# Performance work log

Hardware: AMD Instinct MI355X
Metric: run time of the kernel (lower is better)

The kernel has to match this reference:

```python
import jax, jax.numpy as jnp
import numpy as np


def _count_components(img, cls):
    """Count 4-connected components of pixels equal to `cls` in a 2D int map.

    Equivalent to the numba DFS flood fill: each component is counted once.
    Implemented as min-label propagation: seed every in-class pixel with its
    linear index, iterate min over 4-neighbors (same-class only, since
    out-of-class pixels hold the sentinel BIG) until convergence; a component
    root is a pixel whose final label equals its own index.
    """
    H, W = img.shape
    BIG = H * W  # sentinel larger than any pixel index
    mask = img == cls
    idx = jnp.arange(BIG, dtype=jnp.int32).reshape(H, W)
    lab0 = jnp.where(mask, idx, BIG).astype(jnp.int32)

    def cond(state):
        return state[1]

    def body(state):
        lab, _ = state
        p = jnp.pad(lab, 1, constant_values=BIG)
        nmin = jnp.minimum(jnp.minimum(p[:-2, 1:-1], p[2:, 1:-1]),
                           jnp.minimum(p[1:-1, :-2], p[1:-1, 2:]))
        new = jnp.where(mask, jnp.minimum(lab, nmin), BIG)
        return new, jnp.any(new != lab)

    lab, _ = jax.lax.while_loop(cond, body, (lab0, jnp.array(True)))
    # roots: in-class pixels whose propagated label is their own index
    return jnp.sum(mask & (lab == idx)).astype(jnp.float32)


def _counts23(img):
    # component counts for labels 2 and 3 (the only ones the loss uses)
    return _count_components(img, 2), _count_components(img, 3)


def setup_inputs() -> dict:
    key = jax.random.key(0)
    k1, k2 = jax.random.split(key)
    pred = jax.random.normal(k1, (8, 4, 1, 768, 768), dtype=jnp.float32)
    anno = jax.random.randint(k2, (8, 1, 768, 768), 0, 4, dtype=jnp.int32)
    return {"pred": pred, "anno": anno}


def reference(pred, anno):
    # pred: [B, C, 1, H, W], anno: [B, 1, H, W]
    pred_argmax = jnp.argmax(pred, axis=1)[:, 0]  # [B, H, W] (detached semantics)
    anno_map = anno[:, 0]                          # [B, H, W]
    a2, a3 = jax.vmap(_counts23)(anno_map)
    p2, p3 = jax.vmap(_counts23)(pred_argmax)
    term2 = 1.0 - 2.0 * jnp.minimum(p2, a2) / (a2 + p2)
    term3 = 1.0 - 2.0 * jnp.minimum(p3, a3) / (a3 + p3)
    # original sums per-batch terms into connEF, then loss = connEF / 2
    return jnp.sum(term2 + term3) / 2.0
```

## Files before the change

kernel.cpp:

```cpp
#include <hip/hip_runtime.h>

#define W     768
#define PIX   (768*768)
#define NMAPS 16
#define TROWS 6
#define TPX   (TROWS*W)
#define NT    (768/TROWS)
#define NB    (NT-1)
#define NSEG  (TPX/64)
#define NIT   (NSEG/4)
#define CSLOT 16


__device__ __forceinline__ int find_root_p(volatile int* L, int x) {
    int y = L[x] >> 2;
    while (y != x) { x = y; y = L[x] >> 2; }
    return x;
}

__device__ __forceinline__ bool unite_p(int* L, int a, int b, int c) {
    volatile int* Lv = L;
    while (true) {
        a = find_root_p(Lv, a);
        b = find_root_p(Lv, b);
        if (a == b) return false;
        if (a > b) { int t = a; a = b; b = t; }
        int old = atomicMin(&L[b], (a << 2) | c);
        if ((old >> 2) == b) return true;
        b = old >> 2;
    }
}


__global__ __launch_bounds__(256) void fused_k(const float* __restrict__ pred,
                                               const int*   __restrict__ anno,
                                               int* __restrict__ labels,
                                               int* __restrict__ counts, int m0) {
    __shared__ int lab[TPX];
    __shared__ int s2[4], s3[4];

    int mc   = blockIdx.x / NT;
    int t    = blockIdx.x - mc * NT;
    int m    = m0 + mc;
    int tid  = threadIdx.x;
    int wid  = tid >> 6;
    int lane = tid & 63;

    unsigned long long lem = (lane == 63) ? ~0ULL : ((2ULL << lane) - 1);

    int pc[3] = {0, 0, 0};
    int pm[3] = {0, 0, 0};
    int c2 = 0, c3 = 0;

    const int*   asrc = anno + (size_t)m * PIX + (size_t)t * TPX;
    const float* psrc = pred + (size_t)(m < 8 ? 0 : (m - 8)) * 4 * PIX + (size_t)t * TPX;
    bool is_anno = (m < 8);

    int   na = 0;
    float nv0 = 0.f, nv1 = 0.f, nv2 = 0.f, nv3 = 0.f;
    {
        int px = wid * 64 + lane;
        if (is_anno) {
            na = asrc[px];
        } else {
            nv0 = psrc[px];
            nv1 = psrc[(size_t)PIX + px];
            nv2 = psrc[(size_t)2 * PIX + px];
            nv3 = psrc[(size_t)3 * PIX + px];
        }
    }

    #pragma unroll
    for (int it = 0; it < NIT; ++it) {
        int seg = wid + 4 * it;
        int px  = seg * 64 + lane;
        int   ca = na;
        float v0 = nv0, v1 = nv1, v2 = nv2, v3 = nv3;
        if (it + 1 < NIT) {
            int pxn = px + 256;
            if (is_anno) {
                na = asrc[pxn];
            } else {
                nv0 = psrc[pxn];
                nv1 = psrc[(size_t)PIX + pxn];
                nv2 = psrc[(size_t)2 * PIX + pxn];
                nv3 = psrc[(size_t)3 * PIX + pxn];
            }
        }
        int c;
        if (is_anno) {
            c = ca & 3;
        } else {
            c = 0; float bv = v0;
            if (v1 > bv) { bv = v1; c = 1; }
            if (v2 > bv) { bv = v2; c = 2; }
            if (v3 > bv) { bv = v3; c = 3; }
        }
        unsigned long long blo = __ballot(c & 1);
        unsigned long long bhi = __ballot(c & 2);
        unsigned long long dif = ((blo ^ (blo << 1)) | (bhi ^ (bhi << 1))) | 1ULL;
        if (lane == 0) {
            c2 += (int)__popcll(dif & bhi & ~blo);
            c3 += (int)__popcll(dif & bhi &  blo);
        }
        int ms = 63 - __clzll(dif & lem);
        lab[px] = ((seg * 64 + ms) << 2) | c;
        const int sl = it % 3;
        if (it >= 3) {
            if ((c & 2) && c == pc[sl]) {
                int mx = ms > pm[sl] ? ms : pm[sl];
                if (lane == mx && unite_p(lab, px - W, px, c)) {
                    if (c == 2) c2--; else c3--;
                }
            }
        }
        pc[sl] = c; pm[sl] = ms;
    }
    __syncthreads();

    if (tid < TROWS * 11) {
        int row = tid / 11, j = tid % 11;
        int px  = row * W + (j + 1) * 64;
        int v = lab[px], c = v & 3;
        if (c & 2) {
            int vl = lab[px - 1];
            if ((vl & 3) == c && unite_p(lab, px - 1, px, c)) {
                if (c == 2) c2--; else c3--;
            }
        }
    }
    __syncthreads();

    int lbase = t * TPX;
    int* gl = labels + (size_t)mc * PIX + lbase;
    #pragma unroll
    for (int q = 0; q < 6; ++q) {
        int it  = (q < 3) ? q : (NIT - 6 + q);
        int seg = wid + 4 * it;
        int px  = seg * 64 + lane;
        int v   = lab[px];
        int c   = v & 3;
        int r   = px;
        if (c & 2) r = find_root_p(lab, px);
        int rl = __shfl_up(r, 1);
        gl[px] = ((lbase + r) << 2) | c;
        if ((c & 2) && (lane == 0 || rl != r))
            gl[r] = ((lbase + r) << 2) | c;
    }
    for (int off = 32; off; off >>= 1) {
        c2 += __shfl_down(c2, off, 64);
        c3 += __shfl_down(c3, off, 64);
    }
    if (lane == 0) { s2[wid] = c2; s3[wid] = c3; }
    __syncthreads();
    if (tid == 0) {
        int t2 = s2[0] + s2[1] + s2[2] + s2[3];
        int t3 = s3[0] + s3[1] + s3[2] + s3[3];
        if (t2) atomicAdd(&counts[(m * 2 + 0) * CSLOT], t2);
        if (t3) atomicAdd(&counts[(m * 2 + 1) * CSLOT], t3);
    }
}

__global__ __launch_bounds__(256) void boundary_k(int* __restrict__ labels,
                                                  int* __restrict__ counts, int m0) {
    __shared__ int s2[4], s3[4];
    const int HM = NB * (W / 2);
    int i    = blockIdx.x * 256 + threadIdx.x;
    int mc   = blockIdx.y;
    int m    = m0 + mc;
    int lane = threadIdx.x & 63;

    int m2 = 0, m3 = 0;
    if (i < HM) {
        int b   = i / (W / 2);
        int col = (i - b * (W / 2)) * 2;
        int* L  = labels + (size_t)mc * PIX;
        int p1  = b * TPX + (TROWS - 1) * W + col;
        int p2  = p1 + W;
        int2 va = *(const int2*)&L[p1];
        int2 vb = *(const int2*)&L[p2];
        int pay = __shfl_up(va.y, 1), pby = __shfl_up(vb.y, 1);
        int c0 = va.x & 3;
        if (c0 == (vb.x & 3) && (c0 & 2)) {
            bool red = (lane > 0) && (pay == va.x) && (pby == vb.x);
            if (!red && unite_p(L, p1, p2, c0)) { if (c0 == 2) m2++; else m3++; }
        }
        int c1 = va.y & 3;
        if (c1 == (vb.y & 3) && (c1 & 2)) {
            bool red = (va.x == va.y) && (vb.x == vb.y);
            if (!red && unite_p(L, p1 + 1, p2 + 1, c1)) { if (c1 == 2) m2++; else m3++; }
        }
    }
    for (int off = 32; off; off >>= 1) {
        m2 += __shfl_down(m2, off, 64);
        m3 += __shfl_down(m3, off, 64);
    }
    int wid = threadIdx.x >> 6;
    if (lane == 0) { s2[wid] = m2; s3[wid] = m3; }
    __syncthreads();
    if (threadIdx.x == 0) {
        int t2 = s2[0] + s2[1] + s2[2] + s2[3];
        int t3 = s3[0] + s3[1] + s3[2] + s3[3];
        if (t2) atomicSub(&counts[(m * 2 + 0) * CSLOT], t2);
        if (t3) atomicSub(&counts[(m * 2 + 1) * CSLOT], t3);
    }
}

__global__ void final_k(const int* __restrict__ counts, float* __restrict__ out) {
    float s = 0.0f;
    for (int b = 0; b < 8; ++b) {
        float a2 = (float)counts[(b * 2 + 0) * CSLOT];
        float a3 = (float)counts[(b * 2 + 1) * CSLOT];
        float p2 = (float)counts[((8 + b) * 2 + 0) * CSLOT];
        float p3 = (float)counts[((8 + b) * 2 + 1) * CSLOT];
        float t2 = 1.0f - 2.0f * fminf(p2, a2) / (a2 + p2);
        float t3 = 1.0f - 2.0f * fminf(p3, a3) / (a3 + p3);
        s += t2 + t3;
    }
    out[0] = 0.5f * s;
}


extern "C" void kernel_launch(void* const* d_in, const int* in_sizes, int n_in,
                              void* d_out, int out_size, void* d_ws, size_t ws_size,
                              hipStream_t stream) {
    const float* pred = (const float*)d_in[0];
    const int*   anno = (const int*)d_in[1];
    float* out = (float*)d_out;

    int* counts = (int*)d_ws;
    char* base  = (char*)d_ws + 4096;

    const size_t per_map = (size_t)PIX * 4;
    size_t avail = (ws_size > 4096) ? ws_size - 4096 : 0;
    int K = (int)(avail / per_map);
    if (K > NMAPS) K = NMAPS;
    if (K < 1)     K = 1;

    hipMemsetAsync(counts, 0, 32 * CSLOT * sizeof(int), stream);

    const int HM = NB * (W / 2);
    for (int m0 = 0; m0 < NMAPS; m0 += K) {
        int nm = NMAPS - m0; if (nm > K) nm = K;
        int* labels = (int*)base;
        fused_k   <<<dim3(nm * NT), 256, 0, stream>>>(pred, anno, labels, counts, m0);
        boundary_k<<<dim3((HM + 255) / 256, nm), 256, 0, stream>>>(labels, counts, m0);
    }
    final_k<<<1, 1, 0, stream>>>(counts, out);
}
```

Before: 59.51 us.

## Remap fused CCL tile so each lane handles two pixels in 128-wide row strips

The fused labeling kernel now runs 384 threads, one wave per 128-pixel column strip. Each lane loads two adjacent pixels per row with int2/float2 vector loads and iterates down the 6 rows. Run-start detection combines two ballots per pair, and vertical unions now link consecutive rows within the same wave, with no 3-slot history. The change aims to widen memory accesses, halve the number of ballot iterations and reduce seam unions (5 per row instead of 11). It adds more complex run-boundary logic, and the two-pixels-per-lane indexing is a possible source of correctness bugs.

```diff
diff --git a/kernel.cpp b/kernel.cpp
--- a/kernel.cpp
+++ b/kernel.cpp
@@ -7,8 +7,7 @@
 #define TPX   (TROWS*W)
 #define NT    (768/TROWS)
 #define NB    (NT-1)
-#define NSEG  (TPX/64)
-#define NIT   (NSEG/4)
+#define SW    128
 #define CSLOT 16
 
 
@@ -32,12 +31,12 @@
 }
 
 
-__global__ __launch_bounds__(256) void fused_k(const float* __restrict__ pred,
+__global__ __launch_bounds__(384) void fused_k(const float* __restrict__ pred,
                                                const int*   __restrict__ anno,
                                                int* __restrict__ labels,
                                                int* __restrict__ counts, int m0) {
     __shared__ int lab[TPX];
-    __shared__ int s2[4], s3[4];
+    __shared__ int s2[6], s3[6];
 
     int mc   = blockIdx.x / NT;
     int t    = blockIdx.x - mc * NT;
@@ -47,80 +46,100 @@
     int lane = tid & 63;
 
     unsigned long long lem = (lane == 63) ? ~0ULL : ((2ULL << lane) - 1);
-
-    int pc[3] = {0, 0, 0};
-    int pm[3] = {0, 0, 0};
+    unsigned long long ltm = lem ^ (1ULL << lane);
+
+    int pc0 = 0, pc1 = 0;
+    int pr0 = 0, pr1 = 0;
     int c2 = 0, c3 = 0;
 
     const int*   asrc = anno + (size_t)m * PIX + (size_t)t * TPX;
     const float* psrc = pred + (size_t)(m < 8 ? 0 : (m - 8)) * 4 * PIX + (size_t)t * TPX;
     bool is_anno = (m < 8);
 
-    int   na = 0;
-    float nv0 = 0.f, nv1 = 0.f, nv2 = 0.f, nv3 = 0.f;
-    {
-        int px = wid * 64 + lane;
+    int sp = wid * SW + 2 * lane;
+
+    int2   na = make_int2(0, 0);
+    float2 nv0 = {0,0}, nv1 = {0,0}, nv2 = {0,0}, nv3 = {0,0};
+    if (is_anno) {
+        na = *(const int2*)&asrc[sp];
+    } else {
+        const float2* f = (const float2*)psrc;
+        int i2 = sp >> 1;
+        nv0 = f[i2];
+        nv1 = f[(PIX >> 1) + i2];
+        nv2 = f[2 * (PIX >> 1) + i2];
+        nv3 = f[3 * (PIX >> 1) + i2];
+    }
+
+    #pragma unroll
+    for (int r = 0; r < TROWS; ++r) {
+        int tb  = r * W + wid * SW;
+        int px0 = tb + 2 * lane;
+        int2   ca = na;
+        float2 v0 = nv0, v1 = nv1, v2 = nv2, v3 = nv3;
+        if (r + 1 < TROWS) {
+            int spn = px0 + W;
+            if (is_anno) {
+                na = *(const int2*)&asrc[spn];
+            } else {
+                const float2* f = (const float2*)psrc;
+                int i2 = spn >> 1;
+                nv0 = f[i2];
+                nv1 = f[(PIX >> 1) + i2];
+                nv2 = f[2 * (PIX >> 1) + i2];
+                nv3 = f[3 * (PIX >> 1) + i2];
+            }
+        }
+        int c0, c1;
         if (is_anno) {
-            na = asrc[px];
+            c0 = ca.x & 3; c1 = ca.y & 3;
         } else {
-            nv0 = psrc[px];
-            nv1 = psrc[(size_t)PIX + px];
-            nv2 = psrc[(size_t)2 * PIX + px];
-            nv3 = psrc[(size_t)3 * PIX + px];
-        }
-    }
-
-    #pragma unroll
-    for (int it = 0; it < NIT; ++it) {
-        int seg = wid + 4 * it;
-        int px  = seg * 64 + lane;
-        int   ca = na;
-        float v0 = nv0, v1 = nv1, v2 = nv2, v3 = nv3;
-        if (it + 1 < NIT) {
-            int pxn = px + 256;
-            if (is_anno) {
-                na = asrc[pxn];
-            } else {
-                nv0 = psrc[pxn];
-                nv1 = psrc[(size_t)PIX + pxn];
-                nv2 = psrc[(size_t)2 * PIX + pxn];
-                nv3 = psrc[(size_t)3 * PIX + pxn];
-            }
-        }
-        int c;
-        if (is_anno) {
-            c = ca & 3;
-        } else {
-            c = 0; float bv = v0;
-            if (v1 > bv) { bv = v1; c = 1; }
-            if (v2 > bv) { bv = v2; c = 2; }
-            if (v3 > bv) { bv = v3; c = 3; }
-        }
-        unsigned long long blo = __ballot(c & 1);
-        unsigned long long bhi = __ballot(c & 2);
-        unsigned long long dif = ((blo ^ (blo << 1)) | (bhi ^ (bhi << 1))) | 1ULL;
+            {   float bv = v0.x; c0 = 0;
+                if (v1.x > bv) { bv = v1.x; c0 = 1; }
+                if (v2.x > bv) { bv = v2.x; c0 = 2; }
+                if (v3.x > bv) { bv = v3.x; c0 = 3; } }
+            {   float bv = v0.y; c1 = 0;
+                if (v1.y > bv) { bv = v1.y; c1 = 1; }
+                if (v2.y > bv) { bv = v2.y; c1 = 2; }
+                if (v3.y > bv) { bv = v3.y; c1 = 3; } }
+        }
+        unsigned long long blo0 = __ballot(c0 & 1);
+        unsigned long long bhi0 = __ballot(c0 & 2);
+        unsigned long long blo1 = __ballot(c1 & 1);
+        unsigned long long bhi1 = __ballot(c1 & 2);
+        unsigned long long d0 = ((blo0 ^ (blo1 << 1)) | (bhi0 ^ (bhi1 << 1))) | 1ULL;
+        unsigned long long d1 = (blo1 ^ blo0) | (bhi1 ^ bhi0);
         if (lane == 0) {
-            c2 += (int)__popcll(dif & bhi & ~blo);
-            c3 += (int)__popcll(dif & bhi &  blo);
-        }
-        int ms = 63 - __clzll(dif & lem);
-        lab[px] = ((seg * 64 + ms) << 2) | c;
-        const int sl = it % 3;
-        if (it >= 3) {
-            if ((c & 2) && c == pc[sl]) {
-                int mx = ms > pm[sl] ? ms : pm[sl];
-                if (lane == mx && unite_p(lab, px - W, px, c)) {
-                    if (c == 2) c2--; else c3--;
+            c2 += (int)__popcll(d0 & bhi0 & ~blo0) + (int)__popcll(d1 & bhi1 & ~blo1);
+            c3 += (int)__popcll(d0 & bhi0 &  blo0) + (int)__popcll(d1 & bhi1 &  blo1);
+        }
+        int rs0 = 2 * (63 - __clzll(d0 & lem));
+        unsigned long long mm = d1 & ltm;
+        if (mm) { int q = 2 * (63 - __clzll(mm)) + 1; if (q > rs0) rs0 = q; }
+        int rs1 = ((d1 >> lane) & 1) ? 2 * lane + 1 : rs0;
+        *(int2*)&lab[px0] = make_int2(((tb + rs0) << 2) | c0,
+                                      ((tb + rs1) << 2) | c1);
+        if (r > 0) {
+            if ((c0 & 2) && c0 == pc0) {
+                int mx = rs0 > pr0 ? rs0 : pr0;
+                if (mx == 2 * lane && unite_p(lab, px0 - W, px0, c0)) {
+                    if (c0 == 2) c2--; else c3--;
                 }
             }
-        }
-        pc[sl] = c; pm[sl] = ms;
-    }
-    __syncthreads();
-
-    if (tid < TROWS * 11) {
-        int row = tid / 11, j = tid % 11;
-        int px  = row * W + (j + 1) * 64;
+            if ((c1 & 2) && c1 == pc1) {
+                int mx = rs1 > pr1 ? rs1 : pr1;
+                if (mx == 2 * lane + 1 && unite_p(lab, px0 + 1 - W, px0 + 1, c1)) {
+                    if (c1 == 2) c2--; else c3--;
+                }
+            }
+        }
+        pc0 = c0; pc1 = c1; pr0 = rs0; pr1 = rs1;
+    }
+    __syncthreads();
+
+    if (tid < TROWS * 5) {
+        int row = tid / 5, s = tid % 5 + 1;
+        int px  = row * W + s * SW;
         int v = lab[px], c = v & 3;
         if (c & 2) {
             int vl = lab[px - 1];
@@ -134,18 +153,20 @@
     int lbase = t * TPX;
     int* gl = labels + (size_t)mc * PIX + lbase;
     #pragma unroll
-    for (int q = 0; q < 6; ++q) {
-        int it  = (q < 3) ? q : (NIT - 6 + q);
-        int seg = wid + 4 * it;
-        int px  = seg * 64 + lane;
-        int v   = lab[px];
-        int c   = v & 3;
-        int r   = px;
-        if (c & 2) r = find_root_p(lab, px);
-        int rl = __shfl_up(r, 1);
-        gl[px] = ((lbase + r) << 2) | c;
-        if ((c & 2) && (lane == 0 || rl != r))
-            gl[r] = ((lbase + r) << 2) | c;
+    for (int q = 0; q < 2; ++q) {
+        int r   = q ? (TROWS - 1) : 0;
+        int px0 = r * W + wid * SW + 2 * lane;
+        int v0 = lab[px0], v1 = lab[px0 + 1];
+        int c0 = v0 & 3, c1 = v1 & 3;
+        int r0 = (c0 & 2) ? find_root_p(lab, px0)     : px0;
+        int r1 = (c1 & 2) ? find_root_p(lab, px0 + 1) : px0 + 1;
+        *(int2*)&gl[px0] = make_int2(((lbase + r0) << 2) | c0,
+                                     ((lbase + r1) << 2) | c1);
+        int rl = __shfl_up(r1, 1);
+        if ((c0 & 2) && (lane == 0 || rl != r0))
+            gl[r0] = ((lbase + r0) << 2) | c0;
+        if ((c1 & 2) && r1 != r0)
+            gl[r1] = ((lbase + r1) << 2) | c1;
     }
     for (int off = 32; off; off >>= 1) {
         c2 += __shfl_down(c2, off, 64);
@@ -154,8 +175,8 @@
     if (lane == 0) { s2[wid] = c2; s3[wid] = c3; }
     __syncthreads();
     if (tid == 0) {
-        int t2 = s2[0] + s2[1] + s2[2] + s2[3];
-        int t3 = s3[0] + s3[1] + s3[2] + s3[3];
+        int t2 = s2[0] + s2[1] + s2[2] + s2[3] + s2[4] + s2[5];
+        int t3 = s3[0] + s3[1] + s3[2] + s3[3] + s3[4] + s3[5];
         if (t2) atomicAdd(&counts[(m * 2 + 0) * CSLOT], t2);
         if (t3) atomicAdd(&counts[(m * 2 + 1) * CSLOT], t3);
     }
@@ -243,7 +264,7 @@
     for (int m0 = 0; m0 < NMAPS; m0 += K) {
         int nm = NMAPS - m0; if (nm > K) nm = K;
         int* labels = (int*)base;
-        fused_k   <<<dim3(nm * NT), 256, 0, stream>>>(pred, anno, labels, counts, m0);
+        fused_k   <<<dim3(nm * NT), 384, 0, stream>>>(pred, anno, labels, counts, m0);
         boundary_k<<<dim3((HM + 255) / 256, nm), 256, 0, stream>>>(labels, counts, m0);
     }
     final_k<<<1, 1, 0, stream>>>(counts, out);
```

Result: slower. 62.90 us (+5.7%).

## Split fused kernel into specialized anno and pred kernels with different tile heights

Applied to the files above, without the earlier changes.

Replaces the single fused labeling kernel, which branched per map between the int annotation path and the 4-channel float argmax path, with two specialized kernels. The annotation kernel keeps 6-row tiles, while the prediction kernel uses 3-row tiles so more blocks share the heavier 4-channel loads. The boundary merge kernel is templated on tile height. Maps are now processed in two separate batches of at most 8, which doubles the launches when the workspace could hold all 16 maps, and 3-row pred tiles add more boundary rows to merge.

```diff
diff --git a/kernel.cpp b/kernel.cpp
--- a/kernel.cpp
+++ b/kernel.cpp
@@ -2,14 +2,16 @@
 
 #define W     768
 #define PIX   (768*768)
-#define NMAPS 16
-#define TROWS 6
-#define TPX   (TROWS*W)
-#define NT    (768/TROWS)
-#define NB    (NT-1)
-#define NSEG  (TPX/64)
-#define NIT   (NSEG/4)
 #define CSLOT 16
+
+#define TR_A  6
+#define TPX_A (TR_A*W)
+#define NT_A  (768/TR_A)
+#define NIT_A 18
+#define TR_P  3
+#define TPX_P (TR_P*W)
+#define NT_P  (768/TR_P)
+#define NIT_P 9
 
 
 __device__ __forceinline__ int find_root_p(volatile int* L, int x) {
@@ -32,92 +34,11 @@
 }
 
 
-__global__ __launch_bounds__(256) void fused_k(const float* __restrict__ pred,
-                                               const int*   __restrict__ anno,
-                                               int* __restrict__ labels,
-                                               int* __restrict__ counts, int m0) {
-    __shared__ int lab[TPX];
-    __shared__ int s2[4], s3[4];
-
-    int mc   = blockIdx.x / NT;
-    int t    = blockIdx.x - mc * NT;
-    int m    = m0 + mc;
-    int tid  = threadIdx.x;
-    int wid  = tid >> 6;
-    int lane = tid & 63;
-
-    unsigned long long lem = (lane == 63) ? ~0ULL : ((2ULL << lane) - 1);
-
-    int pc[3] = {0, 0, 0};
-    int pm[3] = {0, 0, 0};
-    int c2 = 0, c3 = 0;
-
-    const int*   asrc = anno + (size_t)m * PIX + (size_t)t * TPX;
-    const float* psrc = pred + (size_t)(m < 8 ? 0 : (m - 8)) * 4 * PIX + (size_t)t * TPX;
-    bool is_anno = (m < 8);
-
-    int   na = 0;
-    float nv0 = 0.f, nv1 = 0.f, nv2 = 0.f, nv3 = 0.f;
-    {
-        int px = wid * 64 + lane;
-        if (is_anno) {
-            na = asrc[px];
-        } else {
-            nv0 = psrc[px];
-            nv1 = psrc[(size_t)PIX + px];
-            nv2 = psrc[(size_t)2 * PIX + px];
-            nv3 = psrc[(size_t)3 * PIX + px];
-        }
-    }
-
-    #pragma unroll
-    for (int it = 0; it < NIT; ++it) {
-        int seg = wid + 4 * it;
-        int px  = seg * 64 + lane;
-        int   ca = na;
-        float v0 = nv0, v1 = nv1, v2 = nv2, v3 = nv3;
-        if (it + 1 < NIT) {
-            int pxn = px + 256;
-            if (is_anno) {
-                na = asrc[pxn];
-            } else {
-                nv0 = psrc[pxn];
-                nv1 = psrc[(size_t)PIX + pxn];
-                nv2 = psrc[(size_t)2 * PIX + pxn];
-                nv3 = psrc[(size_t)3 * PIX + pxn];
-            }
-        }
-        int c;
-        if (is_anno) {
-            c = ca & 3;
-        } else {
-            c = 0; float bv = v0;
-            if (v1 > bv) { bv = v1; c = 1; }
-            if (v2 > bv) { bv = v2; c = 2; }
-            if (v3 > bv) { bv = v3; c = 3; }
-        }
-        unsigned long long blo = __ballot(c & 1);
-        unsigned long long bhi = __ballot(c & 2);
-        unsigned long long dif = ((blo ^ (blo << 1)) | (bhi ^ (bhi << 1))) | 1ULL;
-        if (lane == 0) {
-            c2 += (int)__popcll(dif & bhi & ~blo);
-            c3 += (int)__popcll(dif & bhi &  blo);
-        }
-        int ms = 63 - __clzll(dif & lem);
-        lab[px] = ((seg * 64 + ms) << 2) | c;
-        const int sl = it % 3;
-        if (it >= 3) {
-            if ((c & 2) && c == pc[sl]) {
-                int mx = ms > pm[sl] ? ms : pm[sl];
-                if (lane == mx && unite_p(lab, px - W, px, c)) {
-                    if (c == 2) c2--; else c3--;
-                }
-            }
-        }
-        pc[sl] = c; pm[sl] = ms;
-    }
-    __syncthreads();
-
+template <int TROWS, int NIT>
+__device__ __forceinline__ void tile_tail(int* lab, int* labels, int* counts,
+                                          int mc, int t, int m,
+                                          int tid, int wid, int lane,
+                                          int c2, int c3, int* s2, int* s3) {
     if (tid < TROWS * 11) {
         int row = tid / 11, j = tid % 11;
         int px  = row * W + (j + 1) * 64;
@@ -131,7 +52,7 @@
     }
     __syncthreads();
 
-    int lbase = t * TPX;
+    int lbase = t * (TROWS * W);
     int* gl = labels + (size_t)mc * PIX + lbase;
     #pragma unroll
     for (int q = 0; q < 6; ++q) {
@@ -161,9 +82,125 @@
     }
 }
 
+__global__ __launch_bounds__(256) void anno_k(const int* __restrict__ anno,
+                                              int* __restrict__ labels,
+                                              int* __restrict__ counts, int m0) {
+    __shared__ int lab[TPX_A];
+    __shared__ int s2[4], s3[4];
+    int mc   = blockIdx.x / NT_A;
+    int t    = blockIdx.x - mc * NT_A;
+    int m    = m0 + mc;
+    int tid  = threadIdx.x;
+    int wid  = tid >> 6;
+    int lane = tid & 63;
+    unsigned long long lem = (lane == 63) ? ~0ULL : ((2ULL << lane) - 1);
+
+    int pc[3] = {0,0,0}, pm[3] = {0,0,0};
+    int c2 = 0, c3 = 0;
+    const int* asrc = anno + (size_t)m * PIX + (size_t)t * TPX_A;
+
+    int na = asrc[wid * 64 + lane];
+    #pragma unroll
+    for (int it = 0; it < NIT_A; ++it) {
+        int seg = wid + 4 * it;
+        int px  = seg * 64 + lane;
+        int ca  = na;
+        if (it + 1 < NIT_A) na = asrc[px + 256];
+        int c = ca & 3;
+        unsigned long long blo = __ballot(c & 1);
+        unsigned long long bhi = __ballot(c & 2);
+        unsigned long long dif = ((blo ^ (blo << 1)) | (bhi ^ (bhi << 1))) | 1ULL;
+        if (lane == 0) {
+            c2 += (int)__popcll(dif & bhi & ~blo);
+            c3 += (int)__popcll(dif & bhi &  blo);
+        }
+        int ms = 63 - __clzll(dif & lem);
+        lab[px] = ((seg * 64 + ms) << 2) | c;
+        const int sl = it % 3;
+        if (it >= 3) {
+            if ((c & 2) && c == pc[sl]) {
+                int mx = ms > pm[sl] ? ms : pm[sl];
+                if (lane == mx && unite_p(lab, px - W, px, c)) {
+                    if (c == 2) c2--; else c3--;
+                }
+            }
+        }
+        pc[sl] = c; pm[sl] = ms;
+    }
+    __syncthreads();
+    tile_tail<TR_A, NIT_A>(lab, labels, counts, mc, t, m, tid, wid, lane, c2, c3, s2, s3);
+}
+
+__global__ __launch_bounds__(256) void pred_k(const float* __restrict__ pred,
+                                              int* __restrict__ labels,
+                                              int* __restrict__ counts, int m0) {
+    __shared__ int lab[TPX_P];
+    __shared__ int s2[4], s3[4];
+    int mc   = blockIdx.x / NT_P;
+    int t    = blockIdx.x - mc * NT_P;
+    int m    = m0 + mc;
+    int tid  = threadIdx.x;
+    int wid  = tid >> 6;
+    int lane = tid & 63;
+    unsigned long long lem = (lane == 63) ? ~0ULL : ((2ULL << lane) - 1);
+
+    int pc[3] = {0,0,0}, pm[3] = {0,0,0};
+    int c2 = 0, c3 = 0;
+    const float* psrc = pred + (size_t)(m - 8) * 4 * PIX + (size_t)t * TPX_P;
+
+    float nv0, nv1, nv2, nv3;
+    {
+        int px = wid * 64 + lane;
+        nv0 = psrc[px];
+        nv1 = psrc[(size_t)PIX + px];
+        nv2 = psrc[(size_t)2 * PIX + px];
+        nv3 = psrc[(size_t)3 * PIX + px];
+    }
+    #pragma unroll
+    for (int it = 0; it < NIT_P; ++it) {
+        int seg = wid + 4 * it;
+        int px  = seg * 64 + lane;
+        float v0 = nv0, v1 = nv1, v2 = nv2, v3 = nv3;
+        if (it + 1 < NIT_P) {
+            int pxn = px + 256;
+            nv0 = psrc[pxn];
+            nv1 = psrc[(size_t)PIX + pxn];
+            nv2 = psrc[(size_t)2 * PIX + pxn];
+            nv3 = psrc[(size_t)3 * PIX + pxn];
+        }
+        int c = 0; float bv = v0;
+        if (v1 > bv) { bv = v1; c = 1; }
+        if (v2 > bv) { bv = v2; c = 2; }
+        if (v3 > bv) { bv = v3; c = 3; }
+        unsigned long long blo = __ballot(c & 1);
+        unsigned long long bhi = __ballot(c & 2);
+        unsigned long long dif = ((blo ^ (blo << 1)) | (bhi ^ (bhi << 1))) | 1ULL;
+        if (lane == 0) {
+            c2 += (int)__popcll(dif & bhi & ~blo);
+            c3 += (int)__popcll(dif & bhi &  blo);
+        }
+        int ms = 63 - __clzll(dif & lem);
+        lab[px] = ((seg * 64 + ms) << 2) | c;
+        const int sl = it % 3;
+        if (it >= 3) {
+            if ((c & 2) && c == pc[sl]) {
+                int mx = ms > pm[sl] ? ms : pm[sl];
+                if (lane == mx && unite_p(lab, px - W, px, c)) {
+                    if (c == 2) c2--; else c3--;
+                }
+            }
+        }
+        pc[sl] = c; pm[sl] = ms;
+    }
+    __syncthreads();
+    tile_tail<TR_P, NIT_P>(lab, labels, counts, mc, t, m, tid, wid, lane, c2, c3, s2, s3);
+}
+
+template <int TROWS>
 __global__ __launch_bounds__(256) void boundary_k(int* __restrict__ labels,
                                                   int* __restrict__ counts, int m0) {
     __shared__ int s2[4], s3[4];
+    const int NB = 768 / TROWS - 1;
     const int HM = NB * (W / 2);
     int i    = blockIdx.x * 256 + threadIdx.x;
     int mc   = blockIdx.y;
@@ -175,7 +212,7 @@
         int b   = i / (W / 2);
         int col = (i - b * (W / 2)) * 2;
         int* L  = labels + (size_t)mc * PIX;
-        int p1  = b * TPX + (TROWS - 1) * W + col;
+        int p1  = b * (TROWS * W) + (TROWS - 1) * W + col;
         int p2  = p1 + W;
         int2 va = *(const int2*)&L[p1];
         int2 vb = *(const int2*)&L[p2];
@@ -230,21 +267,30 @@
 
     int* counts = (int*)d_ws;
     char* base  = (char*)d_ws + 4096;
+    int* labels = (int*)base;
 
     const size_t per_map = (size_t)PIX * 4;
     size_t avail = (ws_size > 4096) ? ws_size - 4096 : 0;
     int K = (int)(avail / per_map);
-    if (K > NMAPS) K = NMAPS;
-    if (K < 1)     K = 1;
+    if (K >= 8) K = 8;
+    else if (K >= 4) K = 4;
+    else if (K >= 2) K = 2;
+    else K = 1;
 
     hipMemsetAsync(counts, 0, 32 * CSLOT * sizeof(int), stream);
 
-    const int HM = NB * (W / 2);
-    for (int m0 = 0; m0 < NMAPS; m0 += K) {
-        int nm = NMAPS - m0; if (nm > K) nm = K;
-        int* labels = (int*)base;
-        fused_k   <<<dim3(nm * NT), 256, 0, stream>>>(pred, anno, labels, counts, m0);
-        boundary_k<<<dim3((HM + 255) / 256, nm), 256, 0, stream>>>(labels, counts, m0);
+    const int HM_A = (768 / TR_A - 1) * (W / 2);
+    const int HM_P = (768 / TR_P - 1) * (W / 2);
+
+    for (int m0 = 0; m0 < 8; m0 += K) {
+        int nm = 8 - m0; if (nm > K) nm = K;
+        anno_k<<<dim3(nm * NT_A), 256, 0, stream>>>(anno, labels, counts, m0);
+        boundary_k<TR_A><<<dim3((HM_A + 255) / 256, nm), 256, 0, stream>>>(labels, counts, m0);
+    }
+    for (int m0 = 8; m0 < 16; m0 += K) {
+        int nm = 16 - m0; if (nm > K) nm = K;
+        pred_k<<<dim3(nm * NT_P), 256, 0, stream>>>(pred, labels, counts, m0);
+        boundary_k<TR_P><<<dim3((HM_P + 255) / 256, nm), 256, 0, stream>>>(labels, counts, m0);
     }
     final_k<<<1, 1, 0, stream>>>(counts, out);
 }
```

Result: slower. 89.04 us (+49.6%).
